# Performance work log

Hardware: AMD Instinct MI355X
Metric: run time of the kernel (lower is better)

The kernel has to match this reference:

```python
import jax, jax.numpy as jnp
import numpy as np

EPS = 1e-10


def setup_inputs() -> dict:
    key = jax.random.key(0)
    k1, k2 = jax.random.split(key)
    b, p, c = 8192, 512, 1000
    x = jax.random.normal(k1, (b, p), dtype=jnp.float32)
    means = jax.random.normal(k2, (c, p), dtype=jnp.float32)
    return {"x": x, "means": means}


def reference(x, means):
    # scale factor: L2 norm of the first class mean (np.linalg.norm(mean_logits_np[0]))
    scale = jnp.sqrt(jnp.sum(means[0] ** 2))
    # L2-normalize x along feature dim, then rescale to ||means[0]||
    xn = x / (jnp.linalg.norm(x, axis=1, keepdims=True) + EPS) * scale
    # logits = -||xn - mu_c||^2, expanded as -(||xn||^2 - 2 xn.mu + ||mu||^2)
    # avoids materializing the (b, num_classes, p) intermediate of the original
    x_sq = jnp.sum(xn * xn, axis=1, keepdims=True)          # (b, 1)
    m_sq = jnp.sum(means * means, axis=1)                   # (c,)
    cross = jnp.einsum('bp,cp->bc', xn, means)              # (b, c)
    logits = -(x_sq - 2.0 * cross + m_sq[None, :])
    return logits
```

## Files before the change

kernel.cpp:

```cpp
#include <hip/hip_runtime.h>
#include <hip/hip_bf16.h>
#include <stdint.h>

typedef __bf16 bf16x8 __attribute__((ext_vector_type(8)));
typedef float  f32x4  __attribute__((ext_vector_type(4)));
typedef __attribute__((address_space(1))) const void* gptr_t;
typedef __attribute__((address_space(3))) void*       sptr_t;

#define B_ROWS 8192
#define C_CLS  1000
#define C_PAD  1024
#define P_DIM  512
#define EPS    1e-10f

#define WS_MEANS_BF 0
#define WS_MSQ      1048576
#define WS_XN_BF    1052672
#define WS_XSQ      9441280

__device__ __forceinline__ float dot8(float4 a, float4 b) {
    return a.x * a.x + a.y * a.y + a.z * a.z + a.w * a.w
         + b.x * b.x + b.y * b.y + b.z * b.z + b.w * b.w;
}

__global__ __launch_bounds__(256) void prep_k(const float* __restrict__ x,
                                              const float* __restrict__ means,
                                              __hip_bfloat16* __restrict__ means_bf,
                                              float* __restrict__ m_sq,
                                              __hip_bfloat16* __restrict__ xn_bf,
                                              float* __restrict__ x_sq) {
    const int w = threadIdx.x >> 6;
    const int l = threadIdx.x & 63;
    const int bid = blockIdx.x;

    if (bid < B_ROWS / 4) {
        const int row = bid * 4 + w;
        const float4* m0 = (const float4*)means;
        float4 ma = m0[l * 2];
        float4 mb = m0[l * 2 + 1];
        float ms = dot8(ma, mb);
        const float4* xr = (const float4*)(x + (size_t)row * P_DIM);
        float4 a = xr[l * 2];
        float4 b = xr[l * 2 + 1];
        float s = dot8(a, b);
        #pragma unroll
        for (int off = 32; off > 0; off >>= 1) {
            ms += __shfl_down(ms, off);
            s  += __shfl_down(s, off);
        }
        ms = __shfl(ms, 0);
        s  = __shfl(s, 0);
        float scale = sqrtf(ms);
        float norm  = sqrtf(s);
        float sc    = scale / (norm + EPS);
        alignas(16) __hip_bfloat16 tmp[8];
        tmp[0] = __float2bfloat16(a.x * sc); tmp[1] = __float2bfloat16(a.y * sc);
        tmp[2] = __float2bfloat16(a.z * sc); tmp[3] = __float2bfloat16(a.w * sc);
        tmp[4] = __float2bfloat16(b.x * sc); tmp[5] = __float2bfloat16(b.y * sc);
        tmp[6] = __float2bfloat16(b.z * sc); tmp[7] = __float2bfloat16(b.w * sc);
        *(uint4*)(xn_bf + (size_t)row * P_DIM + l * 8) = *(const uint4*)tmp;
        if (l == 0) {
            float sn = sc * norm;
            x_sq[row] = sn * sn;
        }
    } else {
        const int c = (bid - B_ROWS / 4) * 4 + w;
        if (c < C_CLS) {
            const float4* mr = (const float4*)(means + (size_t)c * P_DIM);
            float4 a = mr[l * 2];
            float4 b = mr[l * 2 + 1];
            float s = dot8(a, b);
            alignas(16) __hip_bfloat16 tmp[8];
            tmp[0] = __float2bfloat16(a.x); tmp[1] = __float2bfloat16(a.y);
            tmp[2] = __float2bfloat16(a.z); tmp[3] = __float2bfloat16(a.w);
            tmp[4] = __float2bfloat16(b.x); tmp[5] = __float2bfloat16(b.y);
            tmp[6] = __float2bfloat16(b.z); tmp[7] = __float2bfloat16(b.w);
            *(uint4*)(means_bf + (size_t)c * P_DIM + l * 8) = *(const uint4*)tmp;
            #pragma unroll
            for (int off = 32; off > 0; off >>= 1) s += __shfl_down(s, off);
            if (l == 0) m_sq[c] = s;
        } else {
            uint4 z = {0u, 0u, 0u, 0u};
            *(uint4*)(means_bf + (size_t)c * P_DIM + l * 8) = z;
            if (l == 0) m_sq[c] = 0.0f;
        }
    }
}

__global__ __launch_bounds__(256, 4) void gemm_k(const __hip_bfloat16* __restrict__ A,
                                                 const __hip_bfloat16* __restrict__ B,
                                                 const float* __restrict__ x_sq,
                                                 const float* __restrict__ m_sq,
                                                 float* __restrict__ out) {
    __shared__ alignas(16) char lds[24576];
    const int t   = threadIdx.x;
    const int w   = t >> 6;
    const int l   = t & 63;
    const int q   = l >> 4;
    const int m16 = l & 15;

    const int n_blk   = blockIdx.x;
    const int xcd     = n_blk & 7;
    const int within  = n_blk >> 3;
    const int brow    = xcd * 16 + (within & 15);
    const int bcol    = within >> 4;

    f32x4 acc[4][2];
    #pragma unroll
    for (int i = 0; i < 4; ++i)
        #pragma unroll
        for (int j = 0; j < 2; ++j) {
            f32x4 z = {0.f, 0.f, 0.f, 0.f};
            acc[i][j] = z;
        }

    const char* Abase = (const char*)A + (size_t)(brow * 64)  * (P_DIM * 2);
    const char* Bbase = (const char*)B + (size_t)(bcol * 128) * (P_DIM * 2);

    const int swz = (m16 & 7) << 4;

    for (int k0 = 0; k0 < P_DIM; k0 += 64) {
        #pragma unroll
        for (int r = 0; r < 6; ++r) {
            const int wbase = r * 4096 + w * 1024;
            const int o     = wbase + l * 16;
            const char* g;
            if (r < 2) {
                const int row = o >> 7;
                const int c   = (o >> 4) & 7;
                g = Abase + (size_t)row * (P_DIM * 2) + k0 * 2 + ((c ^ (row & 7)) << 4);
            } else {
                const int o2  = o - 8192;
                const int row = o2 >> 7;
                const int c   = (o2 >> 4) & 7;
                g = Bbase + (size_t)row * (P_DIM * 2) + k0 * 2 + ((c ^ (row & 7)) << 4);
            }
            __builtin_amdgcn_global_load_lds((gptr_t)g, (sptr_t)(lds + wbase), 16, 0, 0);
        }
        __syncthreads();

        #pragma unroll
        for (int s = 0; s < 2; ++s) {
            const int kb = s * 64 + q * 16;
            bf16x8 af[4], bfr[2];
            #pragma unroll
            for (int i = 0; i < 4; ++i) {
                const int m = i * 16 + m16;
                af[i] = *(const bf16x8*)(lds + m * 128 + (kb ^ swz));
            }
            #pragma unroll
            for (int j = 0; j < 2; ++j) {
                const int nn = w * 32 + j * 16 + m16;
                bfr[j] = *(const bf16x8*)(lds + 8192 + nn * 128 + (kb ^ swz));
            }
            #pragma unroll
            for (int i = 0; i < 4; ++i)
                #pragma unroll
                for (int j = 0; j < 2; ++j)
                    acc[i][j] = __builtin_amdgcn_mfma_f32_16x16x32_bf16(af[i], bfr[j], acc[i][j], 0, 0, 0);
        }
        __syncthreads();
    }

    const int rowbase = brow * 64;
    const int colbase = bcol * 128 + w * 32;
    float msq[2];
    #pragma unroll
    for (int j = 0; j < 2; ++j) {
        const int col = colbase + j * 16 + m16;
        msq[j] = (col < C_CLS) ? m_sq[col] : 0.0f;
    }
    #pragma unroll
    for (int i = 0; i < 4; ++i) {
        #pragma unroll
        for (int reg = 0; reg < 4; ++reg) {
            const int row = rowbase + i * 16 + q * 4 + reg;
            const float xsq = x_sq[row];
            #pragma unroll
            for (int j = 0; j < 2; ++j) {
                const int col = colbase + j * 16 + m16;
                if (col < C_CLS) {
                    out[(size_t)row * C_CLS + col] = 2.0f * acc[i][j][reg] - xsq - msq[j];
                }
            }
        }
    }
}

extern "C" void kernel_launch(void* const* d_in, const int* in_sizes, int n_in,
                              void* d_out, int out_size, void* d_ws, size_t ws_size,
                              hipStream_t stream) {
    const float* x     = (const float*)d_in[0];
    const float* means = (const float*)d_in[1];
    float* out = (float*)d_out;
    char* ws = (char*)d_ws;

    __hip_bfloat16* means_bf = (__hip_bfloat16*)(ws + WS_MEANS_BF);
    float*          m_sq     = (float*)(ws + WS_MSQ);
    __hip_bfloat16* xn_bf    = (__hip_bfloat16*)(ws + WS_XN_BF);
    float*          x_sq     = (float*)(ws + WS_XSQ);

    prep_k<<<B_ROWS / 4 + C_PAD / 4, 256, 0, stream>>>(x, means, means_bf, m_sq, xn_bf, x_sq);
    gemm_k<<<1024, 256, 0, stream>>>(xn_bf, means_bf, x_sq, m_sq, out);
}
```

Before: 89.32 us.

## Fuse x normalization and bf16 conversion into the GEMM A-tile load

Removes the separate pass that normalized x and wrote a bf16 copy to workspace. Each GEMM block now computes row norms for its 64 rows from fp32 x, then loads fp32 A tiles directly, scales and converts them to bf16 and stores them swizzled into LDS. This cuts a full write and re-read of the bf16 activations. The cost is that each x row is reread and renormalized by every column block (8 of them), and the A tile uses register loads instead of async global-to-LDS loads.

```diff
diff --git a/kernel.cpp b/kernel.cpp
--- a/kernel.cpp
+++ b/kernel.cpp
@@ -15,95 +15,79 @@
 
 #define WS_MEANS_BF 0
 #define WS_MSQ      1048576
-#define WS_XN_BF    1052672
-#define WS_XSQ      9441280
 
 __device__ __forceinline__ float dot8(float4 a, float4 b) {
     return a.x * a.x + a.y * a.y + a.z * a.z + a.w * a.w
          + b.x * b.x + b.y * b.y + b.z * b.z + b.w * b.w;
 }
 
-__global__ __launch_bounds__(256) void prep_k(const float* __restrict__ x,
-                                              const float* __restrict__ means,
-                                              __hip_bfloat16* __restrict__ means_bf,
-                                              float* __restrict__ m_sq,
-                                              __hip_bfloat16* __restrict__ xn_bf,
-                                              float* __restrict__ x_sq) {
+__global__ __launch_bounds__(256) void prep_means(const float* __restrict__ means,
+                                                  __hip_bfloat16* __restrict__ means_bf,
+                                                  float* __restrict__ m_sq) {
     const int w = threadIdx.x >> 6;
     const int l = threadIdx.x & 63;
-    const int bid = blockIdx.x;
-
-    if (bid < B_ROWS / 4) {
-        const int row = bid * 4 + w;
-        const float4* m0 = (const float4*)means;
-        float4 ma = m0[l * 2];
-        float4 mb = m0[l * 2 + 1];
-        float ms = dot8(ma, mb);
-        const float4* xr = (const float4*)(x + (size_t)row * P_DIM);
-        float4 a = xr[l * 2];
-        float4 b = xr[l * 2 + 1];
+    const int c = blockIdx.x * 4 + w;
+    if (c < C_CLS) {
+        const float4* mr = (const float4*)(means + (size_t)c * P_DIM);
+        float4 a = mr[l * 2];
+        float4 b = mr[l * 2 + 1];
         float s = dot8(a, b);
+        alignas(16) __hip_bfloat16 tmp[8];
+        tmp[0] = __float2bfloat16(a.x); tmp[1] = __float2bfloat16(a.y);
+        tmp[2] = __float2bfloat16(a.z); tmp[3] = __float2bfloat16(a.w);
+        tmp[4] = __float2bfloat16(b.x); tmp[5] = __float2bfloat16(b.y);
+        tmp[6] = __float2bfloat16(b.z); tmp[7] = __float2bfloat16(b.w);
+        *(uint4*)(means_bf + (size_t)c * P_DIM + l * 8) = *(const uint4*)tmp;
         #pragma unroll
-        for (int off = 32; off > 0; off >>= 1) {
-            ms += __shfl_down(ms, off);
-            s  += __shfl_down(s, off);
-        }
-        ms = __shfl(ms, 0);
-        s  = __shfl(s, 0);
-        float scale = sqrtf(ms);
-        float norm  = sqrtf(s);
-        float sc    = scale / (norm + EPS);
-        alignas(16) __hip_bfloat16 tmp[8];
-        tmp[0] = __float2bfloat16(a.x * sc); tmp[1] = __float2bfloat16(a.y * sc);
-        tmp[2] = __float2bfloat16(a.z * sc); tmp[3] = __float2bfloat16(a.w * sc);
-        tmp[4] = __float2bfloat16(b.x * sc); tmp[5] = __float2bfloat16(b.y * sc);
-        tmp[6] = __float2bfloat16(b.z * sc); tmp[7] = __float2bfloat16(b.w * sc);
-        *(uint4*)(xn_bf + (size_t)row * P_DIM + l * 8) = *(const uint4*)tmp;
-        if (l == 0) {
-            float sn = sc * norm;
-            x_sq[row] = sn * sn;
-        }
+        for (int off = 32; off > 0; off >>= 1) s += __shfl_down(s, off);
+        if (l == 0) m_sq[c] = s;
     } else {
-        const int c = (bid - B_ROWS / 4) * 4 + w;
-        if (c < C_CLS) {
-            const float4* mr = (const float4*)(means + (size_t)c * P_DIM);
-            float4 a = mr[l * 2];
-            float4 b = mr[l * 2 + 1];
-            float s = dot8(a, b);
-            alignas(16) __hip_bfloat16 tmp[8];
-            tmp[0] = __float2bfloat16(a.x); tmp[1] = __float2bfloat16(a.y);
-            tmp[2] = __float2bfloat16(a.z); tmp[3] = __float2bfloat16(a.w);
-            tmp[4] = __float2bfloat16(b.x); tmp[5] = __float2bfloat16(b.y);
-            tmp[6] = __float2bfloat16(b.z); tmp[7] = __float2bfloat16(b.w);
-            *(uint4*)(means_bf + (size_t)c * P_DIM + l * 8) = *(const uint4*)tmp;
-            #pragma unroll
-            for (int off = 32; off > 0; off >>= 1) s += __shfl_down(s, off);
-            if (l == 0) m_sq[c] = s;
-        } else {
-            uint4 z = {0u, 0u, 0u, 0u};
-            *(uint4*)(means_bf + (size_t)c * P_DIM + l * 8) = z;
-            if (l == 0) m_sq[c] = 0.0f;
-        }
+        uint4 z = {0u, 0u, 0u, 0u};
+        *(uint4*)(means_bf + (size_t)c * P_DIM + l * 8) = z;
+        if (l == 0) m_sq[c] = 0.0f;
     }
 }
 
-__global__ __launch_bounds__(256, 4) void gemm_k(const __hip_bfloat16* __restrict__ A,
-                                                 const __hip_bfloat16* __restrict__ B,
-                                                 const float* __restrict__ x_sq,
+__global__ __launch_bounds__(256, 4) void gemm_k(const float* __restrict__ X,
+                                                 const __hip_bfloat16* __restrict__ Bm,
                                                  const float* __restrict__ m_sq,
                                                  float* __restrict__ out) {
     __shared__ alignas(16) char lds[24576];
+    __shared__ float xsq_lds[64];
     const int t   = threadIdx.x;
     const int w   = t >> 6;
     const int l   = t & 63;
     const int q   = l >> 4;
     const int m16 = l & 15;
 
-    const int n_blk   = blockIdx.x;
-    const int xcd     = n_blk & 7;
-    const int within  = n_blk >> 3;
-    const int brow    = xcd * 16 + (within & 15);
-    const int bcol    = within >> 4;
+    const int n_blk  = blockIdx.x;
+    const int xcd    = n_blk & 7;
+    const int within = n_blk >> 3;
+    const int brow   = xcd * 16 + (within & 15);
+    const int bcol   = within >> 4;
+
+    const int rowbase = brow * 64;
+
+    const int prow = t >> 2;
+    const int pseg = t & 3;
+    float scl;
+    {
+        const float4* xr = (const float4*)(X + (size_t)(rowbase + prow) * P_DIM + pseg * 128);
+        float s = 0.f;
+        #pragma unroll 8
+        for (int i = 0; i < 32; ++i) {
+            float4 v = xr[i];
+            s += v.x * v.x + v.y * v.y + v.z * v.z + v.w * v.w;
+        }
+        s += __shfl_xor(s, 1);
+        s += __shfl_xor(s, 2);
+        const float norm = sqrtf(s);
+        scl = sqrtf(m_sq[0]) / (norm + EPS);
+        if (pseg == 0) {
+            const float sn = scl * norm;
+            xsq_lds[prow] = sn * sn;
+        }
+    }
 
     f32x4 acc[4][2];
     #pragma unroll
@@ -114,29 +98,39 @@
             acc[i][j] = z;
         }
 
-    const char* Abase = (const char*)A + (size_t)(brow * 64)  * (P_DIM * 2);
-    const char* Bbase = (const char*)B + (size_t)(bcol * 128) * (P_DIM * 2);
+    const float* Arow  = X + (size_t)(rowbase + prow) * P_DIM;
+    const char*  Bbase = (const char*)Bm + (size_t)(bcol * 128) * (P_DIM * 2);
 
     const int swz = (m16 & 7) << 4;
+    const int sc0 = (((pseg * 2)     ^ (prow & 7)) << 4);
+    const int sc1 = (((pseg * 2 + 1) ^ (prow & 7)) << 4);
+    char* const awr = lds + prow * 128;
 
     for (int k0 = 0; k0 < P_DIM; k0 += 64) {
+        const float* ak = Arow + k0 + pseg * 16;
+        float4 f0 = ((const float4*)ak)[0];
+        float4 f1 = ((const float4*)ak)[1];
+        float4 f2 = ((const float4*)ak)[2];
+        float4 f3 = ((const float4*)ak)[3];
         #pragma unroll
-        for (int r = 0; r < 6; ++r) {
-            const int wbase = r * 4096 + w * 1024;
-            const int o     = wbase + l * 16;
-            const char* g;
-            if (r < 2) {
-                const int row = o >> 7;
-                const int c   = (o >> 4) & 7;
-                g = Abase + (size_t)row * (P_DIM * 2) + k0 * 2 + ((c ^ (row & 7)) << 4);
-            } else {
-                const int o2  = o - 8192;
-                const int row = o2 >> 7;
-                const int c   = (o2 >> 4) & 7;
-                g = Bbase + (size_t)row * (P_DIM * 2) + k0 * 2 + ((c ^ (row & 7)) << 4);
-            }
-            __builtin_amdgcn_global_load_lds((gptr_t)g, (sptr_t)(lds + wbase), 16, 0, 0);
+        for (int r = 0; r < 4; ++r) {
+            const int o2  = r * 4096 + w * 1024 + l * 16;
+            const int row = o2 >> 7;
+            const int c   = (o2 >> 4) & 7;
+            const char* g = Bbase + (size_t)row * (P_DIM * 2) + k0 * 2 + ((c ^ (row & 7)) << 4);
+            __builtin_amdgcn_global_load_lds((gptr_t)g, (sptr_t)(lds + 8192 + r * 4096 + w * 1024), 16, 0, 0);
         }
+        alignas(16) __hip_bfloat16 tb[16];
+        tb[0]  = __float2bfloat16(f0.x * scl); tb[1]  = __float2bfloat16(f0.y * scl);
+        tb[2]  = __float2bfloat16(f0.z * scl); tb[3]  = __float2bfloat16(f0.w * scl);
+        tb[4]  = __float2bfloat16(f1.x * scl); tb[5]  = __float2bfloat16(f1.y * scl);
+        tb[6]  = __float2bfloat16(f1.z * scl); tb[7]  = __float2bfloat16(f1.w * scl);
+        tb[8]  = __float2bfloat16(f2.x * scl); tb[9]  = __float2bfloat16(f2.y * scl);
+        tb[10] = __float2bfloat16(f2.z * scl); tb[11] = __float2bfloat16(f2.w * scl);
+        tb[12] = __float2bfloat16(f3.x * scl); tb[13] = __float2bfloat16(f3.y * scl);
+        tb[14] = __float2bfloat16(f3.z * scl); tb[15] = __float2bfloat16(f3.w * scl);
+        *(uint4*)(awr + sc0) = ((const uint4*)tb)[0];
+        *(uint4*)(awr + sc1) = ((const uint4*)tb)[1];
         __syncthreads();
 
         #pragma unroll
@@ -162,7 +156,6 @@
         __syncthreads();
     }
 
-    const int rowbase = brow * 64;
     const int colbase = bcol * 128 + w * 32;
     float msq[2];
     #pragma unroll
@@ -174,8 +167,9 @@
     for (int i = 0; i < 4; ++i) {
         #pragma unroll
         for (int reg = 0; reg < 4; ++reg) {
-            const int row = rowbase + i * 16 + q * 4 + reg;
-            const float xsq = x_sq[row];
+            const int lrow = i * 16 + q * 4 + reg;
+            const int row  = rowbase + lrow;
+            const float xsq = xsq_lds[lrow];
             #pragma unroll
             for (int j = 0; j < 2; ++j) {
                 const int col = colbase + j * 16 + m16;
@@ -197,9 +191,7 @@
 
     __hip_bfloat16* means_bf = (__hip_bfloat16*)(ws + WS_MEANS_BF);
     float*          m_sq     = (float*)(ws + WS_MSQ);
-    __hip_bfloat16* xn_bf    = (__hip_bfloat16*)(ws + WS_XN_BF);
-    float*          x_sq     = (float*)(ws + WS_XSQ);
 
-    prep_k<<<B_ROWS / 4 + C_PAD / 4, 256, 0, stream>>>(x, means, means_bf, m_sq, xn_bf, x_sq);
-    gemm_k<<<1024, 256, 0, stream>>>(xn_bf, means_bf, x_sq, m_sq, out);
+    prep_means<<<C_PAD / 4, 256, 0, stream>>>(means, means_bf, m_sq);
+    gemm_k<<<1024, 256, 0, stream>>>(x, means_bf, m_sq, out);
 }
```

Result: slower. 106.1 us (+18.8%).
